# Kernel tuning notes

Measured on AMD Instinct MI355X. Metric: run time of the kernel, lower is better.

The kernel has to match this reference:

```python
import jax, jax.numpy as jnp
import numpy as np

BETA = 0.9
THR = 1.0
B, T, F, H = 64, 256, 1024, 512

# snntorch heaviside spike with ATan surrogate gradient (alpha=2.0, snntorch default)
@jax.custom_vjp
def spike_fn(u):
    return (u > 0).astype(u.dtype)

def _spike_fwd(u):
    return spike_fn(u), u

def _spike_bwd(u, g):
    alpha = 2.0
    grad = (alpha / 2.0) / (1.0 + (jnp.pi / 2.0 * alpha * u) ** 2)
    return (g * grad,)

spike_fn.defvjp(_spike_fwd, _spike_bwd)


def setup_inputs() -> dict:
    key = jax.random.key(0)
    ks = jax.random.split(key, 12)
    s = 0.05
    return {
        "f_f": jax.random.normal(ks[0], (B, T, F), dtype=jnp.float32),
        "seq_len": jnp.full((B,), T, dtype=jnp.int64),
        "Wf": jax.random.normal(ks[1], (H, F), dtype=jnp.float32) * s,
        "bf": jnp.zeros((H,), jnp.float32),
        "W1": jax.random.normal(ks[2], (H, H), dtype=jnp.float32) * s,
        "b1": jnp.zeros((H,), jnp.float32),
        "W2": jax.random.normal(ks[3], (H, H), dtype=jnp.float32) * s,
        "b2": jnp.zeros((H,), jnp.float32),
        "Mw1": jax.random.normal(ks[4], (512, H), dtype=jnp.float32) * s,
        "Mb1": jnp.zeros((512,), jnp.float32),
        "Mw2": jax.random.normal(ks[5], (32, 512), dtype=jnp.float32) * s,
        "Mb2": jnp.zeros((32,), jnp.float32),
        "Mw3": jax.random.normal(ks[6], (1, 32), dtype=jnp.float32) * s,
        "Mb3": jnp.zeros((1,), jnp.float32),
    }


def _forward(f_f, Wf, bf, W1, b1, W2, b2, Mw1, Mb1, Mw2, Mb2, Mw3, Mb3):
    h = f_f @ Wf.T + bf            # [B,T,H] fc_f
    x1 = h @ W1.T + b1             # layer-1 linear drive precomputed (state-independent)

    def step(carry, x1_t):
        m1, m2 = carry
        # snntorch Leaky (subtract reset): reset from previous mem's spike
        r1 = spike_fn(m1 - THR)
        m1 = BETA * m1 + x1_t - r1 * THR
        s1 = spike_fn(m1 - THR)
        x2 = s1 @ W2.T + b2        # layer-2 linear on spikes (dropout=identity, eval)
        r2 = spike_fn(m2 - THR)
        m2 = BETA * m2 + x2 - r2 * THR
        s2 = spike_fn(m2 - THR)
        return (m1, m2), s2

    init = (jnp.zeros((B, H), h.dtype), jnp.zeros((B, H), h.dtype))
    _, spk = jax.lax.scan(step, init, jnp.swapaxes(x1, 0, 1))  # [T,B,H]
    spk = jnp.swapaxes(spk, 0, 1)                              # [B,T,H]

    z = jax.nn.relu(spk @ Mw1.T + Mb1)
    z = z @ Mw2.T + Mb2
    logits = jax.nn.sigmoid((z @ Mw3.T + Mb3).squeeze(-1))     # [B,T]

    # filter: top-(seq_len//16 + 1) mean per clip; seq_len == T for all clips
    k = T // 16 + 1
    topv, _ = jax.lax.top_k(logits, k)
    return jnp.mean(topv, axis=-1)                             # [B]


def reference(f_f, seq_len, Wf, bf, W1, b1, W2, b2, Mw1, Mb1, Mw2, Mb2, Mw3, Mb3):
    return _forward(f_f, Wf, bf, W1, b1, W2, b2, Mw1, Mb1, Mw2, Mb2, Mw3, Mb3)
```

## Files before the change

kernel.cpp:

```cpp
#include <hip/hip_runtime.h>
#include <math.h>

#define BETA 0.9f
#define THR 1.0f

constexpr int B_ = 64, T_ = 256, F_ = 1024, H_ = 512;
constexpr int M_ = B_ * T_;

typedef float f32x4 __attribute__((ext_vector_type(4)));
typedef short short8 __attribute__((ext_vector_type(8)));
typedef _Float16 half8 __attribute__((ext_vector_type(8)));
typedef unsigned short us4 __attribute__((ext_vector_type(4)));
typedef unsigned short us8 __attribute__((ext_vector_type(8)));
typedef unsigned short ushort_t;

static __device__ __forceinline__ unsigned short f2bf(float x) {
    unsigned b = __builtin_bit_cast(unsigned, x);
    unsigned r = (b + 0x7FFFu + ((b >> 16) & 1u)) >> 16;
    return (unsigned short)r;
}
static __device__ __forceinline__ float bf2f(unsigned short u) {
    unsigned v = ((unsigned)u) << 16;
    return __builtin_bit_cast(float, v);
}
static __device__ __forceinline__ unsigned short f2h(float x) {
    _Float16 h = (_Float16)x;
    return __builtin_bit_cast(unsigned short, h);
}
static __device__ __forceinline__ float h2f(unsigned short u) {
    return (float)__builtin_bit_cast(_Float16, u);
}
static __device__ __forceinline__ int swz(int r) {
    return ((r >> 2) & 3) ^ (r & 3);
}

#define GLDS(srcp, dstp)                                                      \
    __builtin_amdgcn_global_load_lds(                                         \
        (const __attribute__((address_space(1))) unsigned int*)(srcp),        \
        (__attribute__((address_space(3))) unsigned int*)(dstp), 16, 0, 0)

template <int AF32>
__global__ __launch_bounds__(512, 4) void gemm_scan(
    const void* __restrict__ Asrc, const ushort_t* __restrict__ Bp,
    const float* __restrict__ bias, ushort_t* __restrict__ Sout, int K) {
    constexpr int BUF = 20480;
    __shared__ ushort_t lds[2 * BUF];

    const int tid = threadIdx.x;
    const int w = tid >> 6, l = tid & 63;
    const int flat = blockIdx.y * gridDim.x + blockIdx.x;
    const int clip = ((flat >> 6) << 3) | (flat & 7);
    const int strip = (flat >> 3) & 7;
    const int n0 = strip * 64;
    const int m0 = clip * 256;

    f32x4 acc[2][4];
#pragma unroll
    for (int mi = 0; mi < 2; ++mi)
#pragma unroll
        for (int ni = 0; ni < 4; ++ni) acc[mi][ni] = (f32x4){0.f, 0.f, 0.f, 0.f};

    const int c0 = l >> 4;
    const int schunk = (l & 7) ^ ((l >> 3) & 7);

    f32x4 areg[4][2];

    auto stageB = [&](int buf, int k0) {
        const int r = w * 8 + (l >> 3);
        GLDS(Bp + (size_t)(n0 + r) * K + k0 + schunk * 8,
             &lds[buf + 16384 + w * 512]);
    };
    auto stageA16 = [&](int buf, int k0) {
#pragma unroll
        for (int j = 0; j < 4; ++j) {
            const int seg = w * 4 + j;
            const int r = seg * 8 + (l >> 3);
            GLDS((const ushort_t*)Asrc + (size_t)(m0 + r) * K + k0 + schunk * 8,
                 &lds[buf + seg * 512]);
        }
    };
    auto loadA32 = [&](int k0) {
#pragma unroll
        for (int j = 0; j < 4; ++j) {
            const int r = j * 64 + (tid >> 3);
            const float* src =
                (const float*)Asrc + (size_t)(m0 + r) * K + k0 + (tid & 7) * 8;
            areg[j][0] = *(const f32x4*)src;
            areg[j][1] = *(const f32x4*)(src + 4);
        }
    };
    auto writeA32 = [&](int buf) {
#pragma unroll
        for (int j = 0; j < 4; ++j) {
            const int r = j * 64 + (tid >> 3);
            us8 hv;
#pragma unroll
            for (int e = 0; e < 4; ++e) {
                hv[e] = f2h(areg[j][0][e]);
                hv[e + 4] = f2h(areg[j][1][e]);
            }
            const int pos = (tid & 7) ^ (r & 7);
            *(us8*)&lds[buf + r * 64 + pos * 8] = hv;
        }
    };

    const int nt = K / 64;
    if constexpr (AF32) {
        loadA32(0);
        writeA32(0);
    } else {
        stageA16(0, 0);
    }
    stageB(0, 0);

    for (int t = 0; t < nt; ++t) {
        const int cur = (t & 1) * BUF;
        const int nxt = BUF - cur;
        __syncthreads();
        const bool more = (t + 1 < nt);
        if (more) {
            if constexpr (AF32) {
                loadA32((t + 1) * 64);
                stageB(nxt, (t + 1) * 64);
            } else {
                stageA16(nxt, (t + 1) * 64);
                stageB(nxt, (t + 1) * 64);
            }
        }

#pragma unroll
        for (int kh = 0; kh < 2; ++kh) {
            half8 aa[2], bb[4];
            const int q = kh * 4 + c0;
#pragma unroll
            for (int mi = 0; mi < 2; ++mi) {
                const int r = w * 32 + mi * 16 + (l & 15);
                const int off = cur + r * 64 + ((q ^ (l & 7)) * 8);
                aa[mi] = __builtin_bit_cast(half8, *(const short8*)&lds[off]);
            }
#pragma unroll
            for (int ni = 0; ni < 4; ++ni) {
                const int r = ni * 16 + (l & 15);
                const int off = cur + 16384 + r * 64 + ((q ^ (l & 7)) * 8);
                bb[ni] = __builtin_bit_cast(half8, *(const short8*)&lds[off]);
            }
            __builtin_amdgcn_s_setprio(1);
#pragma unroll
            for (int mi = 0; mi < 2; ++mi)
#pragma unroll
                for (int ni = 0; ni < 4; ++ni)
                    acc[mi][ni] = __builtin_amdgcn_mfma_f32_16x16x32_f16(
                        aa[mi], bb[ni], acc[mi][ni], 0, 0, 0);
            __builtin_amdgcn_s_setprio(0);
        }

        if constexpr (AF32) {
            if (more) writeA32(nxt);
        }
    }

    float bv[4];
#pragma unroll
    for (int ni = 0; ni < 4; ++ni) bv[ni] = bias[n0 + ni * 16 + (l & 15)];
#pragma unroll
    for (int mi = 0; mi < 2; ++mi) {
        const int t0 = w * 32 + mi * 16 + ((l >> 4) << 2);
#pragma unroll
        for (int ni = 0; ni < 4; ++ni) {
            const int h = ni * 16 + (l & 15);
#pragma unroll
            for (int r = 0; r < 4; ++r)
                lds[(t0 + r) * 66 + h] = f2h(acc[mi][ni][r] + bv[ni]);
        }
    }
    __syncthreads();

    if (tid < 64) {
        const int h = tid;
        ushort_t* sp = Sout + (size_t)m0 * 512 + n0 + h;
        float m = 0.f;
#pragma unroll 4
        for (int t = 0; t < T_; ++t) {
            const float xv = h2f(lds[t * 66 + h]);
            const float r = (m - THR > 0.f) ? THR : 0.f;
            m = BETA * m + xv - r;
            sp[(size_t)t * 512] = (m - THR > 0.f) ? (ushort_t)0x3C00 : (ushort_t)0;
        }
    }
}

__global__ __launch_bounds__(256) void gemm_mil(
    const ushort_t* __restrict__ Ap, const ushort_t* __restrict__ Bp,
    const float* __restrict__ bias, const float* __restrict__ Uv,
    float* __restrict__ part, int N, int K) {
    constexpr int BUF = 16384;
    __shared__ ushort_t lds[2 * BUF];

    const int tid = threadIdx.x;
    const int w = tid >> 6, l = tid & 63;
    const int flat = blockIdx.y * gridDim.x + blockIdx.x;
    const int mt = ((flat >> 5) << 3) | (flat & 7);
    const int st = (flat >> 3) & 3;
    const int n0 = st * 128;
    const int m0 = mt * 128;
    const int wr = w >> 1, wc = w & 1;

    f32x4 acc[4][4];
#pragma unroll
    for (int mi = 0; mi < 4; ++mi)
#pragma unroll
        for (int ni = 0; ni < 4; ++ni) acc[mi][ni] = (f32x4){0.f, 0.f, 0.f, 0.f};

    const int c0 = l >> 4;
    const int schunk = (l & 7) ^ ((l >> 3) & 7);

    auto stage = [&](int buf, int k0) {
#pragma unroll
        for (int j = 0; j < 8; ++j) {
            const int g = w * 8 + j;
            const int seg = g & 15;
            const int r = seg * 8 + (l >> 3);
            const ushort_t* pl = (g < 16) ? Ap : Bp;
            const int rb = (g < 16) ? m0 : n0;
            GLDS(pl + (size_t)(rb + r) * K + k0 + schunk * 8,
                 &lds[buf + g * 512]);
        }
    };

    const int nt = K / 64;
    stage(0, 0);
    for (int t = 0; t < nt; ++t) {
        const int cur = (t & 1) * BUF;
        const int nxt = BUF - cur;
        __syncthreads();
        if (t + 1 < nt) stage(nxt, (t + 1) * 64);

#pragma unroll
        for (int kh = 0; kh < 2; ++kh) {
            half8 aa[4], bb[4];
            const int q = kh * 4 + c0;
#pragma unroll
            for (int mi = 0; mi < 4; ++mi) {
                const int r = wr * 64 + mi * 16 + (l & 15);
                const int off = cur + r * 64 + ((q ^ (l & 7)) * 8);
                aa[mi] = __builtin_bit_cast(half8, *(const short8*)&lds[off]);
            }
#pragma unroll
            for (int ni = 0; ni < 4; ++ni) {
                const int r = wc * 64 + ni * 16 + (l & 15);
                const int off = cur + 8192 + r * 64 + ((q ^ (l & 7)) * 8);
                bb[ni] = __builtin_bit_cast(half8, *(const short8*)&lds[off]);
            }
            __builtin_amdgcn_s_setprio(1);
#pragma unroll
            for (int mi = 0; mi < 4; ++mi)
#pragma unroll
                for (int ni = 0; ni < 4; ++ni)
                    acc[mi][ni] = __builtin_amdgcn_mfma_f32_16x16x32_f16(
                        aa[mi], bb[ni], acc[mi][ni], 0, 0, 0);
            __builtin_amdgcn_s_setprio(0);
        }
    }

    float bv[4], uc[4];
#pragma unroll
    for (int ni = 0; ni < 4; ++ni) {
        const int col = n0 + wc * 64 + ni * 16 + (l & 15);
        bv[ni] = bias[col];
        uc[ni] = Uv[col];
    }
    const int strip = (n0 >> 6) + wc;
#pragma unroll
    for (int mi = 0; mi < 4; ++mi) {
        float p[4];
#pragma unroll
        for (int r = 0; r < 4; ++r) {
            float s = 0.f;
#pragma unroll
            for (int ni = 0; ni < 4; ++ni)
                s += fmaxf(acc[mi][ni][r] + bv[ni], 0.f) * uc[ni];
            p[r] = s;
        }
#pragma unroll
        for (int off = 1; off <= 8; off <<= 1)
#pragma unroll
            for (int r = 0; r < 4; ++r) p[r] += __shfl_xor(p[r], off);
        if ((l & 15) == 0) {
            const int row0 = m0 + wr * 64 + mi * 16 + ((l >> 4) << 2);
#pragma unroll
            for (int r = 0; r < 4; ++r)
                part[(size_t)strip * M_ + row0 + r] = p[r];
        }
    }
}

__global__ __launch_bounds__(256, 1) void gemm_bf16_wc(
    const ushort_t* __restrict__ Ah, const ushort_t* __restrict__ Al,
    const ushort_t* __restrict__ Bh, const ushort_t* __restrict__ Bl,
    ushort_t* __restrict__ Cout, int N, int K) {
    constexpr int BUF = 32768;
    __shared__ ushort_t lds[2 * BUF];

    const int tid = threadIdx.x;
    const int w = tid >> 6, l = tid & 63;
    const int flat = blockIdx.y * gridDim.x + blockIdx.x;
    const int n0 = (flat % gridDim.x) * 128;
    const int m0 = (flat / gridDim.x) * 128;
    const int wr = w >> 1, wc = w & 1;

    f32x4 acc[4][4];
#pragma unroll
    for (int mi = 0; mi < 4; ++mi)
#pragma unroll
        for (int ni = 0; ni < 4; ++ni) acc[mi][ni] = (f32x4){0.f, 0.f, 0.f, 0.f};

    const int c0 = l >> 4;
    const int schunk = (l & 7) ^ ((l >> 3) & 7);

    auto stage = [&](int buf, int k0) {
#pragma unroll
        for (int j = 0; j < 16; ++j) {
            const int g = w * 16 + j;
            const int p = g >> 4, seg = g & 15;
            const int r = seg * 8 + (l >> 3);
            const ushort_t* pl = (p == 0) ? Ah : (p == 1) ? Al : (p == 2) ? Bh : Bl;
            const int rb = (p < 2) ? m0 : n0;
            GLDS(pl + (size_t)(rb + r) * K + k0 + schunk * 8,
                 &lds[buf + g * 512]);
        }
    };

    const int nt = K / 64;
    stage(0, 0);
    for (int t = 0; t < nt; ++t) {
        const int cur = (t & 1) * BUF;
        const int nxt = BUF - cur;
        __syncthreads();
        if (t + 1 < nt) stage(nxt, (t + 1) * 64);

#pragma unroll
        for (int kh = 0; kh < 2; ++kh) {
            short8 ah[4], al[4], bh[4], bl[4];
            const int q = kh * 4 + c0;
#pragma unroll
            for (int mi = 0; mi < 4; ++mi) {
                const int r = wr * 64 + mi * 16 + (l & 15);
                const int off = r * 64 + ((q ^ (l & 7)) * 8);
                ah[mi] = *(const short8*)&lds[cur + off];
                al[mi] = *(const short8*)&lds[cur + 8192 + off];
            }
#pragma unroll
            for (int ni = 0; ni < 4; ++ni) {
                const int r = wc * 64 + ni * 16 + (l & 15);
                const int off = r * 64 + ((q ^ (l & 7)) * 8);
                bh[ni] = *(const short8*)&lds[cur + 16384 + off];
                bl[ni] = *(const short8*)&lds[cur + 24576 + off];
            }
            __builtin_amdgcn_s_setprio(1);
#pragma unroll
            for (int mi = 0; mi < 4; ++mi)
#pragma unroll
                for (int ni = 0; ni < 4; ++ni) {
                    acc[mi][ni] = __builtin_amdgcn_mfma_f32_16x16x32_bf16(
                        ah[mi], bh[ni], acc[mi][ni], 0, 0, 0);
                    acc[mi][ni] = __builtin_amdgcn_mfma_f32_16x16x32_bf16(
                        ah[mi], bl[ni], acc[mi][ni], 0, 0, 0);
                    acc[mi][ni] = __builtin_amdgcn_mfma_f32_16x16x32_bf16(
                        al[mi], bh[ni], acc[mi][ni], 0, 0, 0);
                }
            __builtin_amdgcn_s_setprio(0);
        }
    }

#pragma unroll
    for (int ni = 0; ni < 4; ++ni) {
        const int col = n0 + wc * 64 + ni * 16 + (l & 15);
#pragma unroll
        for (int mi = 0; mi < 4; ++mi) {
            const int row0 = m0 + wr * 64 + mi * 16 + ((l >> 4) << 2);
#pragma unroll
            for (int r = 0; r < 4; ++r)
                Cout[(size_t)(row0 + r) * N + col] = f2h(acc[mi][ni][r]);
        }
    }
}

__global__ __launch_bounds__(256) void prep_small(
    const float* __restrict__ W1, const float* __restrict__ W2,
    const float* __restrict__ Mw1, const float* __restrict__ bfv,
    const float* __restrict__ b1, const float* __restrict__ Mw2,
    const float* __restrict__ Mb2, const float* __restrict__ Mw3,
    const float* __restrict__ Mb3, const float* __restrict__ Wf,
    ushort_t* __restrict__ w1h, ushort_t* __restrict__ w1l,
    ushort_t* __restrict__ w2f, ushort_t* __restrict__ m1f,
    float* __restrict__ bc, float* __restrict__ uc,
    ushort_t* __restrict__ wfTh, ushort_t* __restrict__ wfTl) {
    __shared__ float tile[32][33];
    const int blk = blockIdx.x;
    const int tid = threadIdx.x;
    if (blk < 256) {
        const int i = blk * 256 + tid;
        f32x4 v = ((const f32x4*)W1)[i];
        us4 h, ll;
#pragma unroll
        for (int e = 0; e < 4; ++e) {
            const unsigned short hb = f2bf(v[e]);
            h[e] = hb;
            ll[e] = f2bf(v[e] - bf2f(hb));
        }
        ((us4*)w1h)[i] = h;
        ((us4*)w1l)[i] = ll;
    } else if (blk < 512) {
        const int i = (blk - 256) * 256 + tid;
        f32x4 v = ((const f32x4*)W2)[i];
        us4 h;
#pragma unroll
        for (int e = 0; e < 4; ++e) h[e] = f2h(v[e]);
        ((us4*)w2f)[i] = h;
    } else if (blk < 768) {
        const int i = (blk - 512) * 256 + tid;
        f32x4 v = ((const f32x4*)Mw1)[i];
        us4 h;
#pragma unroll
        for (int e = 0; e < 4; ++e) h[e] = f2h(v[e]);
        ((us4*)m1f)[i] = h;
    } else if (blk < 896) {
        const int w = tid >> 6, l = tid & 63;
        const int j = (blk - 768) * 4 + w;
        const float* row = W1 + (size_t)j * 512;
        float a = 0.f;
#pragma unroll
        for (int i = 0; i < 8; ++i) a += row[l + i * 64] * bfv[l + i * 64];
#pragma unroll
        for (int off = 32; off >= 1; off >>= 1) a += __shfl_xor(a, off);
        if (l == 0) bc[j] = a + b1[j];
    } else if (blk < 898) {
        const int j = (blk - 896) * 256 + tid;
        float a = 0.f;
        for (int i = 0; i < 32; ++i) a += Mw3[i] * Mw2[(size_t)i * 512 + j];
        uc[j] = a;
        if (j == 0) {
            float c = Mb3[0];
            for (int i = 0; i < 32; ++i) c += Mw3[i] * Mb2[i];
            uc[512] = c;
        }
    } else {
        const int idx = blk - 898;
        const int k0 = (idx & 31) * 32;
        const int i0 = (idx >> 5) * 32;
        const int tx = tid & 31;
        const int ty = tid >> 5;
#pragma unroll
        for (int e = 0; e < 4; ++e) {
            const int i = ty + e * 8;
            tile[i][tx] = Wf[(size_t)(i0 + i) * 1024 + k0 + tx];
        }
        __syncthreads();
#pragma unroll
        for (int e = 0; e < 4; ++e) {
            const int kk = ty + e * 8;
            const float v = tile[tx][kk];
            const unsigned short h = f2bf(v);
            wfTh[(size_t)(k0 + kk) * 512 + i0 + tx] = h;
            wfTl[(size_t)(k0 + kk) * 512 + i0 + tx] = f2bf(v - bf2f(h));
        }
    }
}

__global__ __launch_bounds__(64) void tail_topk(const float* __restrict__ part,
                                                const float* __restrict__ uc,
                                                float* __restrict__ out) {
    const int b = blockIdx.x;
    const int lane = threadIdx.x;
    const float c = uc[512];
    float v[4];
#pragma unroll
    for (int i = 0; i < 4; ++i) {
        const int row = b * T_ + lane + i * 64;
        float a = 0.f;
#pragma unroll
        for (int s = 0; s < 8; ++s) a += part[(size_t)s * M_ + row];
        v[i] = a + c;
    }
    float sum = 0.f;
    for (int iter = 0; iter < 17; ++iter) {
        float mv = v[0];
        int mslot = 0;
#pragma unroll
        for (int i = 1; i < 4; ++i)
            if (v[i] > mv) { mv = v[i]; mslot = i; }
        float bv = mv;
        int bl = lane, bs = mslot;
#pragma unroll
        for (int off = 32; off >= 1; off >>= 1) {
            const float ov = __shfl_xor(bv, off);
            const int ol = __shfl_xor(bl, off);
            const int os = __shfl_xor(bs, off);
            if (ov > bv || (ov == bv && ol < bl)) { bv = ov; bl = ol; bs = os; }
        }
        sum += 1.f / (1.f + expf(-bv));
        if (lane == bl) v[bs] = -1e30f;
    }
    if (lane == 0) out[b] = sum * (1.f / 17.f);
}

extern "C" void kernel_launch(void* const* d_in, const int* in_sizes, int n_in,
                              void* d_out, int out_size, void* d_ws, size_t ws_size,
                              hipStream_t stream) {
    const float* f_f = (const float*)d_in[0];
    const float* Wf  = (const float*)d_in[2];
    const float* bf  = (const float*)d_in[3];
    const float* W1  = (const float*)d_in[4];
    const float* b1  = (const float*)d_in[5];
    const float* W2  = (const float*)d_in[6];
    const float* b2  = (const float*)d_in[7];
    const float* Mw1 = (const float*)d_in[8];
    const float* Mb1 = (const float*)d_in[9];
    const float* Mw2 = (const float*)d_in[10];
    const float* Mb2 = (const float*)d_in[11];
    const float* Mw3 = (const float*)d_in[12];
    const float* Mb3 = (const float*)d_in[13];
    float* out = (float*)d_out;

    char* ws = (char*)d_ws;
    const size_t NE = (size_t)M_ * H_;
    ushort_t* sbuf1 = (ushort_t*)ws;
    ushort_t* sbuf2 = sbuf1 + NE;
    ushort_t* w1h = sbuf2 + NE;
    ushort_t* w1l = w1h + 262144;
    ushort_t* w2f = w1l + 262144;
    ushort_t* m1f = w2f + 262144;
    ushort_t* wfTh = m1f + 262144;
    ushort_t* wfTl = wfTh + 524288;
    ushort_t* wcf = wfTl + 524288;
    float* bc = (float*)(wcf + 524288);
    float* uc = bc + 512;
    float* part = uc + 513 + 63;

    const dim3 blk(256);

    prep_small<<<dim3(1410), blk, 0, stream>>>(W1, W2, Mw1, bf, b1, Mw2, Mb2,
                                               Mw3, Mb3, Wf, w1h, w1l, w2f,
                                               m1f, bc, uc, wfTh, wfTl);

    gemm_bf16_wc<<<dim3(8, 4), blk, 0, stream>>>(w1h, w1l, wfTh, wfTl, wcf,
                                                 1024, 512);
    gemm_scan<1><<<dim3(8, 64), dim3(512), 0, stream>>>(f_f, wcf, bc, sbuf1,
                                                        1024);
    gemm_scan<0><<<dim3(8, 64), dim3(512), 0, stream>>>(sbuf1, w2f, b2, sbuf2,
                                                        512);
    gemm_mil<<<dim3(4, 128), blk, 0, stream>>>(sbuf2, m1f, Mb1, uc, part,
                                               512, 512);
    tail_topk<<<dim3(B_), dim3(64), 0, stream>>>(part, uc, out);
}
```

Baseline: 111.5 us.

## Triple-buffer gemm_scan K loop with explicit waitcnt and two-ahead prefetch

Replaces the double-buffered LDS pipeline in gemm_scan with a three-stage ring that prefetches two K tiles ahead. Each iteration waits on a partial vmcnt before a raw s_barrier instead of a full __syncthreads, so loads can overlap compute over a longer window. The LDS footprint grows by half, and launch bounds drop to 2 blocks per CU, which lowers occupancy. The scan staging area moves to the third buffer, and a sync is added before it is written.

```diff
diff --git a/kernel.cpp b/kernel.cpp
--- a/kernel.cpp
+++ b/kernel.cpp
@@ -40,11 +40,11 @@
         (__attribute__((address_space(3))) unsigned int*)(dstp), 16, 0, 0)
 
 template <int AF32>
-__global__ __launch_bounds__(512, 4) void gemm_scan(
+__global__ __launch_bounds__(512, 2) void gemm_scan(
     const void* __restrict__ Asrc, const ushort_t* __restrict__ Bp,
     const float* __restrict__ bias, ushort_t* __restrict__ Sout, int K) {
     constexpr int BUF = 20480;
-    __shared__ ushort_t lds[2 * BUF];
+    __shared__ ushort_t lds[3 * BUF];
 
     const int tid = threadIdx.x;
     const int w = tid >> 6, l = tid & 63;
@@ -108,23 +108,42 @@
     if constexpr (AF32) {
         loadA32(0);
         writeA32(0);
+        loadA32(64);
+        writeA32(BUF);
+        stageB(0, 0);
+        stageB(BUF, 64);
     } else {
         stageA16(0, 0);
-    }
-    stageB(0, 0);
+        stageB(0, 0);
+        stageA16(BUF, 64);
+        stageB(BUF, 64);
+    }
 
     for (int t = 0; t < nt; ++t) {
-        const int cur = (t & 1) * BUF;
-        const int nxt = BUF - cur;
-        __syncthreads();
-        const bool more = (t + 1 < nt);
-        if (more) {
+        const int cur = (t % 3) * BUF;
+        const int n2 = ((t + 2) % 3) * BUF;
+        const bool pre = (t + 2 < nt);
+        if constexpr (AF32) {
+            if (t + 1 < nt)
+                asm volatile("s_waitcnt vmcnt(1) lgkmcnt(0)" ::: "memory");
+            else
+                asm volatile("s_waitcnt vmcnt(0) lgkmcnt(0)" ::: "memory");
+        } else {
+            if (t + 1 < nt)
+                asm volatile("s_waitcnt vmcnt(5)" ::: "memory");
+            else
+                asm volatile("s_waitcnt vmcnt(0)" ::: "memory");
+        }
+        __builtin_amdgcn_s_barrier();
+        __builtin_amdgcn_sched_barrier(0);
+
+        if (pre) {
             if constexpr (AF32) {
-                loadA32((t + 1) * 64);
-                stageB(nxt, (t + 1) * 64);
+                loadA32((t + 2) * 64);
+                stageB(n2, (t + 2) * 64);
             } else {
-                stageA16(nxt, (t + 1) * 64);
-                stageB(nxt, (t + 1) * 64);
+                stageA16(n2, (t + 2) * 64);
+                stageB(n2, (t + 2) * 64);
             }
         }
 
@@ -155,10 +174,13 @@
         }
 
         if constexpr (AF32) {
-            if (more) writeA32(nxt);
-        }
-    }
-
+            if (pre) writeA32(n2);
+        }
+    }
+
+    __syncthreads();
+
+    constexpr int SOFF = 2 * BUF;
     float bv[4];
 #pragma unroll
     for (int ni = 0; ni < 4; ++ni) bv[ni] = bias[n0 + ni * 16 + (l & 15)];
@@ -170,7 +192,7 @@
             const int h = ni * 16 + (l & 15);
 #pragma unroll
             for (int r = 0; r < 4; ++r)
-                lds[(t0 + r) * 66 + h] = f2h(acc[mi][ni][r] + bv[ni]);
+                lds[SOFF + (t0 + r) * 66 + h] = f2h(acc[mi][ni][r] + bv[ni]);
         }
     }
     __syncthreads();
@@ -181,7 +203,7 @@
         float m = 0.f;
 #pragma unroll 4
         for (int t = 0; t < T_; ++t) {
-            const float xv = h2f(lds[t * 66 + h]);
+            const float xv = h2f(lds[SOFF + t * 66 + h]);
             const float r = (m - THR > 0.f) ? THR : 0.f;
             m = BETA * m + xv - r;
             sp[(size_t)t * 512] = (m - THR > 0.f) ? (ushort_t)0x3C00 : (ushort_t)0;
```

Result: slower. 139.8 us (+25.3%).
